# Performance work log

Hardware: AMD Instinct MI355X
Metric: run time of the kernel (lower is better)

The kernel has to match this reference:

```python
import jax, jax.numpy as jnp
import numpy as np

D_MODEL = 1024
N_LAYER = 4
D_INNER = 2048   # expand * d_model
D_STATE = 16
D_CONV = 4
DT_RANK = 64     # ceil(d_model / 16)
B, L = 2, 1024
EPS = 1e-5


def setup_inputs() -> dict:
    key = jax.random.key(0)
    ks = jax.random.split(key, 10)
    nl = N_LAYER
    def nrm(k, shape, s=0.02):
        return jax.random.normal(k, shape, jnp.float32) * s
    A_log = jnp.broadcast_to(jnp.log(jnp.arange(1, D_STATE + 1, dtype=jnp.float32)),
                             (nl, D_INNER, D_STATE)) + jnp.zeros((nl, D_INNER, D_STATE), jnp.float32)
    return {
        "hidden_states": jax.random.normal(ks[0], (B, L, D_MODEL), jnp.float32),
        "in_proj_w": nrm(ks[1], (nl, 2 * D_INNER, D_MODEL)),
        "conv_w": nrm(ks[2], (nl, D_INNER, D_CONV), 0.1),
        "conv_b": nrm(ks[3], (nl, D_INNER), 0.02),
        "x_proj_w": nrm(ks[4], (nl, DT_RANK + 2 * D_STATE, D_INNER)),
        "dt_proj_w": nrm(ks[5], (nl, D_INNER, DT_RANK), DT_RANK ** -0.5),
        "dt_proj_b": jnp.log(jnp.expm1(jax.random.uniform(ks[6], (nl, D_INNER), jnp.float32, 1e-3, 0.1))),
        "A_log": A_log,
        "D": jnp.ones((nl, D_INNER), jnp.float32),
        "out_proj_w": nrm(ks[7], (nl, D_MODEL, D_INNER)),
        "norm_w": jnp.ones((nl, D_MODEL), jnp.float32),
        "norm_b": jnp.zeros((nl, D_MODEL), jnp.float32),
        "normf_w": jnp.ones((D_MODEL,), jnp.float32),
        "normf_b": jnp.zeros((D_MODEL,), jnp.float32),
    }


def _layernorm(x, w, b):
    mu = x.mean(-1, keepdims=True)
    var = ((x - mu) ** 2).mean(-1, keepdims=True)
    return (x - mu) * jax.lax.rsqrt(var + EPS) * w + b


def _mamba(h, iw, cw, cb, xw, dw, db, Alog, Dp, ow):
    Bn, Ln, _ = h.shape
    xz = jnp.einsum('bld,ed->ble', h, iw)          # [B,L,2*d_inner]
    x, z = jnp.split(xz, 2, axis=-1)
    # depthwise causal conv1d over time, kernel size D_CONV
    xp = jnp.pad(x, ((0, 0), (D_CONV - 1, 0), (0, 0)))
    xc = sum(xp[:, k:k + Ln, :] * cw[:, k] for k in range(D_CONV)) + cb
    x = jax.nn.silu(xc)
    dbl = jnp.einsum('bld,ed->ble', x, xw)         # [B,L,dt_rank+2*d_state]
    dt = dbl[..., :DT_RANK]
    Bm = dbl[..., DT_RANK:DT_RANK + D_STATE]
    Cm = dbl[..., DT_RANK + D_STATE:]
    dt = jax.nn.softplus(jnp.einsum('blr,dr->bld', dt, dw) + db)  # [B,L,d_inner]
    A = -jnp.exp(Alog)                              # [d_inner,d_state]

    def step(hc, inp):
        dt_t, B_t, C_t, x_t = inp                   # [B,d],[B,s],[B,s],[B,d]
        dA = jnp.exp(dt_t[:, :, None] * A)
        hc = hc * dA + (dt_t * x_t)[:, :, None] * B_t[:, None, :]
        y_t = jnp.einsum('bds,bs->bd', hc, C_t)
        return hc, y_t

    h0 = jnp.zeros((Bn, D_INNER, D_STATE), x.dtype)
    xs = (dt.transpose(1, 0, 2), Bm.transpose(1, 0, 2),
          Cm.transpose(1, 0, 2), x.transpose(1, 0, 2))
    _, ys = jax.lax.scan(step, h0, xs)              # ys: [L,B,d_inner]
    y = ys.transpose(1, 0, 2) + x * Dp
    y = y * jax.nn.silu(z)
    return jnp.einsum('bld,ed->ble', y, ow)


def reference(hidden_states, in_proj_w, conv_w, conv_b, x_proj_w, dt_proj_w,
              dt_proj_b, A_log, D, out_proj_w, norm_w, norm_b, normf_w, normf_b):
    hs = hidden_states
    residual = None
    for i in range(N_LAYER):
        residual = hs if residual is None else hs + residual
        hs = _layernorm(residual, norm_w[i], norm_b[i])
        hs = _mamba(hs, in_proj_w[i], conv_w[i], conv_b[i], x_proj_w[i],
                    dt_proj_w[i], dt_proj_b[i], A_log[i], D[i], out_proj_w[i])
    residual = hs + residual
    return _layernorm(residual, normf_w, normf_b)
```

## Files before the change

### kernel.cpp

```cpp
#include <hip/hip_runtime.h>
#include <math.h>

#define D_MODEL 1024
#define D_INNER 2048
#define D_STATE 16
#define D_CONV  4
#define DT_RANK 64
#define NB      2
#define LSEQ    1024
#define NROWS   (NB * LSEQ)
#define LN_EPS  1e-5f
#define N_LAYER 4
#define NCHUNK  32
#define TCH     (LSEQ / NCHUNK)

__device__ inline unsigned bfbits(float f) {
    unsigned u = __float_as_uint(f);
    return (u + 0x7fffu + ((u >> 16) & 1u)) >> 16;
}

#define GLOAD_LDS16(gp, lp) \
    __builtin_amdgcn_global_load_lds( \
        (const __attribute__((address_space(1))) void*)(gp), \
        (__attribute__((address_space(3))) void*)(lp), 16, 0, 0)

__device__ inline float wave_sum(float s) {
    #pragma unroll
    for (int m = 1; m < 64; m <<= 1) s += __shfl_xor(s, m, 64);
    return s;
}

__device__ inline void add_ln_body(int row, int tid,
                                   const float* __restrict__ add,
                                   float* __restrict__ residual,
                                   const float* __restrict__ w, const float* __restrict__ b,
                                   void* __restrict__ out, int first, int bf16out,
                                   float* red)
{
    size_t base = (size_t)row * D_MODEL + tid * 4;

    float4 v = *(const float4*)(add + base);
    if (!first) {
        float4 r = *(const float4*)(residual + base);
        v.x += r.x; v.y += r.y; v.z += r.z; v.w += r.w;
    }
    *(float4*)(residual + base) = v;

    float s = v.x + v.y + v.z + v.w;
    s = wave_sum(s);
    if ((tid & 63) == 0) red[tid >> 6] = s;
    __syncthreads();
    float mu = (red[0] + red[1] + red[2] + red[3]) * (1.0f / D_MODEL);

    float dx = v.x - mu, dy = v.y - mu, dz = v.z - mu, dw2 = v.w - mu;
    float s2 = dx*dx + dy*dy + dz*dz + dw2*dw2;
    s2 = wave_sum(s2);
    if ((tid & 63) == 0) red[4 + (tid >> 6)] = s2;
    __syncthreads();
    float var = (red[4] + red[5] + red[6] + red[7]) * (1.0f / D_MODEL);
    float rs = rsqrtf(var + LN_EPS);

    float4 wv = *(const float4*)(w + tid * 4);
    float4 bv = *(const float4*)(b + tid * 4);
    float4 o;
    o.x = dx  * rs * wv.x + bv.x;
    o.y = dy  * rs * wv.y + bv.y;
    o.z = dz  * rs * wv.z + bv.z;
    o.w = dw2 * rs * wv.w + bv.w;
    if (bf16out) {
        ushort4 ov;
        ov.x = (unsigned short)bfbits(o.x);
        ov.y = (unsigned short)bfbits(o.y);
        ov.z = (unsigned short)bfbits(o.z);
        ov.w = (unsigned short)bfbits(o.w);
        *(ushort4*)((unsigned short*)out + base) = ov;
    } else {
        *(float4*)((float*)out + base) = o;
    }
}

__global__ __launch_bounds__(256)
void add_ln_kernel(const float* __restrict__ add, float* __restrict__ residual,
                   const float* __restrict__ w, const float* __restrict__ b,
                   void* __restrict__ out, int first, int bf16out)
{
    __shared__ float red[8];
    add_ln_body(blockIdx.x, threadIdx.x, add, residual, w, b, out, first, bf16out, red);
}

__global__ __launch_bounds__(256)
void f32_to_bf16_kernel(const float* __restrict__ src, unsigned short* __restrict__ dst)
{
    int i = blockIdx.x * 256 + threadIdx.x;
    float4 v = *(const float4*)(src + (size_t)i * 4);
    ushort4 o;
    o.x = (unsigned short)bfbits(v.x);
    o.y = (unsigned short)bfbits(v.y);
    o.z = (unsigned short)bfbits(v.z);
    o.w = (unsigned short)bfbits(v.w);
    *(ushort4*)(dst + (size_t)i * 4) = o;
}

__device__ inline void hl_split4(float4 v, ushort4* h4, ushort4* l4)
{
    ushort4 h, l;
    float f;
    h.x = (unsigned short)bfbits(v.x); f = __uint_as_float((unsigned)h.x << 16); l.x = (unsigned short)bfbits(v.x - f);
    h.y = (unsigned short)bfbits(v.y); f = __uint_as_float((unsigned)h.y << 16); l.y = (unsigned short)bfbits(v.y - f);
    h.z = (unsigned short)bfbits(v.z); f = __uint_as_float((unsigned)h.z << 16); l.z = (unsigned short)bfbits(v.z - f);
    h.w = (unsigned short)bfbits(v.w); f = __uint_as_float((unsigned)h.w << 16); l.w = (unsigned short)bfbits(v.w - f);
    *h4 = h; *l4 = l;
}

__global__ __launch_bounds__(256)
void lnprep_kernel(const float* __restrict__ add, float* __restrict__ residual,
                   const float* __restrict__ w, const float* __restrict__ b,
                   unsigned short* __restrict__ ln_out, int first,
                   const float* __restrict__ iw, unsigned short* __restrict__ wbuf_in,
                   const float* __restrict__ xw, unsigned short* __restrict__ xwh,
                   unsigned short* __restrict__ xwl,
                   const float* __restrict__ dw, unsigned short* __restrict__ dwh,
                   unsigned short* __restrict__ dwl,
                   float* __restrict__ dbl)
{
    __shared__ float red[8];
    int b0 = blockIdx.x;
    int tid = threadIdx.x;
    if (b0 < 2048) {
        add_ln_body(b0, tid, add, residual, w, b, ln_out, first, 1, red);
    } else if (b0 < 6144) {
        int i = (b0 - 2048) * 256 + tid;
        float4 v = *(const float4*)(iw + (size_t)i * 4);
        ushort4 o;
        o.x = (unsigned short)bfbits(v.x);
        o.y = (unsigned short)bfbits(v.y);
        o.z = (unsigned short)bfbits(v.z);
        o.w = (unsigned short)bfbits(v.w);
        *(ushort4*)(wbuf_in + (size_t)i * 4) = o;
    } else if (b0 < 6336) {
        int i = (b0 - 6144) * 256 + tid;
        float4 v = *(const float4*)(xw + (size_t)i * 4);
        hl_split4(v, (ushort4*)(xwh + (size_t)i * 4), (ushort4*)(xwl + (size_t)i * 4));
    } else if (b0 < 6464) {
        int i = (b0 - 6336) * 256 + tid;
        float4 v = *(const float4*)(dw + (size_t)i * 4);
        hl_split4(v, (ushort4*)(dwh + (size_t)i * 4), (ushort4*)(dwl + (size_t)i * 4));
    } else {
        int i = (b0 - 6464) * 256 + tid;
        *(float4*)(dbl + (size_t)i * 4) = make_float4(0.f, 0.f, 0.f, 0.f);
    }
}

using bf16x8 = __attribute__((ext_vector_type(8))) short;
using f32x4  = __attribute__((ext_vector_type(4))) float;

#define BBM 128
#define BBN 128
#define BBK 64

__global__ __launch_bounds__(256)
void gemm_bf16_nt(const unsigned short* __restrict__ A, const unsigned short* __restrict__ Bw,
                  float* __restrict__ C, int M, int N, int K)
{
    __shared__ unsigned short As[BBM * BBK];
    __shared__ unsigned short Bs[BBN * BBK];

    int tid = threadIdx.x;
    int m0 = blockIdx.y * BBM, n0 = blockIdx.x * BBN;
    int lane = tid & 63, w = tid >> 6;
    int wm = (w >> 1) * 64, wn = (w & 1) * 64;
    int lm = lane & 15, q = lane >> 4;

    int lrow8 = lane >> 3;
    int scol  = ((lane & 7) ^ lrow8) * 8;

    f32x4 acc[4][4] = {};

    for (int k0 = 0; k0 < K; k0 += BBK) {
        #pragma unroll
        for (int j = 0; j < 4; ++j) {
            int rbase = w * 32 + j * 8;
            GLOAD_LDS16(A + (size_t)(m0 + rbase + lrow8) * K + k0 + scol,
                        &As[rbase * BBK]);
        }
        #pragma unroll
        for (int j = 0; j < 4; ++j) {
            int rbase = w * 32 + j * 8;
            GLOAD_LDS16(Bw + (size_t)(n0 + rbase + lrow8) * K + k0 + scol,
                        &Bs[rbase * BBK]);
        }
        __syncthreads();
        #pragma unroll
        for (int kk = 0; kk < BBK; kk += 32) {
            bf16x8 af[4], bf[4];
            #pragma unroll
            for (int i = 0; i < 4; ++i) {
                int row = wm + i * 16 + lm;
                int col = (kk + q * 8) ^ ((row & 7) << 3);
                af[i] = *(const bf16x8*)&As[row * BBK + col];
            }
            #pragma unroll
            for (int j = 0; j < 4; ++j) {
                int row = wn + j * 16 + lm;
                int col = (kk + q * 8) ^ ((row & 7) << 3);
                bf[j] = *(const bf16x8*)&Bs[row * BBK + col];
            }
            #pragma unroll
            for (int i = 0; i < 4; ++i)
                #pragma unroll
                for (int j = 0; j < 4; ++j)
                    acc[i][j] = __builtin_amdgcn_mfma_f32_16x16x32_bf16(
                        af[i], bf[j], acc[i][j], 0, 0, 0);
        }
        __syncthreads();
    }

    #pragma unroll
    for (int i = 0; i < 4; ++i)
        #pragma unroll
        for (int j = 0; j < 4; ++j)
            #pragma unroll
            for (int r = 0; r < 4; ++r) {
                int row = m0 + wm + i * 16 + q * 4 + r;
                int col = n0 + wn + j * 16 + lm;
                C[(size_t)row * N + col] = acc[i][j][r];
            }
}

__global__ __launch_bounds__(256)
void xproj_hl(const unsigned short* __restrict__ Ah, const unsigned short* __restrict__ Al,
              const unsigned short* __restrict__ Bh, const unsigned short* __restrict__ Bl,
              float* __restrict__ C)
{
    int tid = threadIdx.x;
    int lane = tid & 63, w = tid >> 6;
    int lm = lane & 15, q = lane >> 4;
    int m0 = blockIdx.x * 32;
    int kb = blockIdx.y * 256;

    int wm = (w & 1) * 16;
    int wn = (w >> 1) * 48;

    size_t arow = (size_t)(m0 + wm + lm) * 2048;

    f32x4 acc[3] = {};

    #pragma unroll 2
    for (int kc = 0; kc < 8; ++kc) {
        int k = kb + kc * 32 + q * 8;
        bf16x8 ah = *(const bf16x8*)&Ah[arow + k];
        bf16x8 al = *(const bf16x8*)&Al[arow + k];
        #pragma unroll
        for (int j = 0; j < 3; ++j) {
            size_t brow = (size_t)(wn + j * 16 + lm) * 2048;
            bf16x8 bh = *(const bf16x8*)&Bh[brow + k];
            bf16x8 bl = *(const bf16x8*)&Bl[brow + k];
            acc[j] = __builtin_amdgcn_mfma_f32_16x16x32_bf16(al, bh, acc[j], 0, 0, 0);
            acc[j] = __builtin_amdgcn_mfma_f32_16x16x32_bf16(ah, bl, acc[j], 0, 0, 0);
            acc[j] = __builtin_amdgcn_mfma_f32_16x16x32_bf16(ah, bh, acc[j], 0, 0, 0);
        }
    }

    #pragma unroll
    for (int j = 0; j < 3; ++j) {
        int col = wn + j * 16 + lm;
        #pragma unroll
        for (int r = 0; r < 4; ++r) {
            int row = m0 + wm + q * 4 + r;
            atomicAdd(&C[(size_t)row * 96 + col], acc[j][r]);
        }
    }
}

__global__ __launch_bounds__(256)
void dtproj_hl(const float* __restrict__ dbl,
               const unsigned short* __restrict__ Bh, const unsigned short* __restrict__ Bl,
               const float* __restrict__ bias, float* __restrict__ dtb)
{
    int tid = threadIdx.x;
    int lane = tid & 63, w = tid >> 6;
    int lm = lane & 15, q = lane >> 4;
    int n0 = blockIdx.x * 128;
    int m0 = blockIdx.y * 64;

    const float* arow = dbl + (size_t)(m0 + w * 16 + lm) * 96;

    f32x4 acc[8] = {};

    #pragma unroll
    for (int kc = 0; kc < 2; ++kc) {
        int k = kc * 32 + q * 8;
        float4 v0 = *(const float4*)(arow + k);
        float4 v1 = *(const float4*)(arow + k + 4);
        float vv[8] = {v0.x, v0.y, v0.z, v0.w, v1.x, v1.y, v1.z, v1.w};
        bf16x8 ah, al;
        #pragma unroll
        for (int s = 0; s < 8; ++s) {
            unsigned hb = bfbits(vv[s]);
            ah[s] = (short)hb;
            al[s] = (short)bfbits(vv[s] - __uint_as_float(hb << 16));
        }
        #pragma unroll
        for (int j = 0; j < 8; ++j) {
            size_t brow = (size_t)(n0 + j * 16 + lm) * 64;
            bf16x8 bh = *(const bf16x8*)&Bh[brow + k];
            bf16x8 bl = *(const bf16x8*)&Bl[brow + k];
            acc[j] = __builtin_amdgcn_mfma_f32_16x16x32_bf16(al, bh, acc[j], 0, 0, 0);
            acc[j] = __builtin_amdgcn_mfma_f32_16x16x32_bf16(ah, bl, acc[j], 0, 0, 0);
            acc[j] = __builtin_amdgcn_mfma_f32_16x16x32_bf16(ah, bh, acc[j], 0, 0, 0);
        }
    }

    #pragma unroll
    for (int j = 0; j < 8; ++j) {
        int col = n0 + j * 16 + lm;
        float bv = bias[col];
        #pragma unroll
        for (int r = 0; r < 4; ++r) {
            int row = m0 + w * 16 + q * 4 + r;
            float v = acc[j][r] + bv;
            v = (v > 20.f) ? v : log1pf(__expf(v));
            dtb[(size_t)row * D_INNER + col] = v;
        }
    }
}

__global__ __launch_bounds__(256)
void conv_silu_kernel(const float* __restrict__ xz, const float* __restrict__ cw,
                      const float* __restrict__ cb, float* __restrict__ xc,
                      unsigned short* __restrict__ xch, unsigned short* __restrict__ xcl)
{
    int idx = blockIdx.x * 256 + threadIdx.x;
    int d  = idx & (D_INNER - 1);
    int t  = (idx >> 11) & (LSEQ - 1);
    int bb = idx >> 21;

    const float* xcol = xz + (size_t)bb * LSEQ * 2 * D_INNER + d;
    float acc = cb[d];
    #pragma unroll
    for (int k = 0; k < D_CONV; ++k) {
        int tt = t + k - (D_CONV - 1);
        if (tt >= 0) acc += xcol[(size_t)tt * 2 * D_INNER] * cw[d * D_CONV + k];
    }
    acc = acc / (1.f + __expf(-acc));
    xc[idx] = acc;
    unsigned hb = bfbits(acc);
    xch[idx] = (unsigned short)hb;
    float hf = __uint_as_float(hb << 16);
    xcl[idx] = (unsigned short)bfbits(acc - hf);
}

#define UNPK4(dst, off, v) { dst[(off)+0]=(v).x; dst[(off)+1]=(v).y; \
                             dst[(off)+2]=(v).z; dst[(off)+3]=(v).w; }

__global__ __launch_bounds__(256)
void scan_pass1(const float* __restrict__ dtb, const float* __restrict__ xc,
                const float* __restrict__ dbl, const float* __restrict__ Alog,
                float* __restrict__ aPbuf, float* __restrict__ bAbuf)
{
    int tid  = threadIdx.x;
    int half = tid & 1;
    int blk  = blockIdx.x;
    int dg   = blk & 15;
    int c    = (blk >> 4) & (NCHUNK - 1);
    int bb   = blk >> 9;
    int d    = dg * 128 + (tid >> 1);

    float A[8];
    {
        const float* pA = Alog + (size_t)d * D_STATE + half * 8;
        float4 v0 = *(const float4*)pA;
        float4 v1 = *(const float4*)(pA + 4);
        A[0] = -__expf(v0.x); A[1] = -__expf(v0.y);
        A[2] = -__expf(v0.z); A[3] = -__expf(v0.w);
        A[4] = -__expf(v1.x); A[5] = -__expf(v1.y);
        A[6] = -__expf(v1.z); A[7] = -__expf(v1.w);
    }

    size_t rowbase = (size_t)bb * LSEQ + (size_t)c * TCH;
    const float* pdt = dtb + rowbase * D_INNER + d;
    const float* pxc = xc  + rowbase * D_INNER + d;
    const float* pbc = dbl + rowbase * 96 + DT_RANK + half * 8;

    float aP[8] = {1.f,1.f,1.f,1.f,1.f,1.f,1.f,1.f};
    float bA[8] = {0.f,0.f,0.f,0.f,0.f,0.f,0.f,0.f};

    float  dtE = pdt[0], xvE = pxc[0];
    float4 BE0 = *(const float4*)pbc;
    float4 BE1 = *(const float4*)(pbc + 4);
    float  dtO = pdt[D_INNER], xvO = pxc[D_INNER];
    float4 BO0 = *(const float4*)(pbc + 96);
    float4 BO1 = *(const float4*)(pbc + 96 + 4);

    const float* qdtE = pdt + 2 * D_INNER;
    const float* qdtO = pdt + 3 * D_INNER;
    const float* qxcE = pxc + 2 * D_INNER;
    const float* qxcO = pxc + 3 * D_INNER;
    const float* qbcE = pbc + 2 * 96;
    const float* qbcO = pbc + 3 * 96;

#define P1_STEP(DT, XV, B0, B1) { \
        float B[8]; UNPK4(B, 0, B0) UNPK4(B, 4, B1) \
        float dtx = (DT) * (XV); \
        _Pragma("unroll") \
        for (int s = 0; s < 8; ++s) { \
            float a = __expf((DT) * A[s]); \
            aP[s] *= a; \
            bA[s] = bA[s] * a + dtx * B[s]; \
        } }

    for (int t = 0; t < TCH - 4; t += 2) {
        float  dtEn = qdtE[0], xvEn = qxcE[0];
        float4 BE0n = *(const float4*)qbcE;
        float4 BE1n = *(const float4*)(qbcE + 4);
        float  dtOn = qdtO[0], xvOn = qxcO[0];
        float4 BO0n = *(const float4*)qbcO;
        float4 BO1n = *(const float4*)(qbcO + 4);
        qdtE += 2 * D_INNER; qdtO += 2 * D_INNER;
        qxcE += 2 * D_INNER; qxcO += 2 * D_INNER;
        qbcE += 192; qbcO += 192;

        P1_STEP(dtE, xvE, BE0, BE1)
        P1_STEP(dtO, xvO, BO0, BO1)

        dtE = dtEn; xvE = xvEn; BE0 = BE0n; BE1 = BE1n;
        dtO = dtOn; xvO = xvOn; BO0 = BO0n; BO1 = BO1n;
    }
    {
        float  dtEn = qdtE[0], xvEn = qxcE[0];
        float4 BE0n = *(const float4*)qbcE;
        float4 BE1n = *(const float4*)(qbcE + 4);
        float  dtOn = qdtO[0], xvOn = qxcO[0];
        float4 BO0n = *(const float4*)qbcO;
        float4 BO1n = *(const float4*)(qbcO + 4);

        P1_STEP(dtE, xvE, BE0, BE1)
        P1_STEP(dtO, xvO, BO0, BO1)

        dtE = dtEn; xvE = xvEn; BE0 = BE0n; BE1 = BE1n;
        dtO = dtOn; xvO = xvOn; BO0 = BO0n; BO1 = BO1n;
    }
    {
        P1_STEP(dtE, xvE, BE0, BE1)
        P1_STEP(dtO, xvO, BO0, BO1)
    }
#undef P1_STEP

    float* pa = aPbuf + ((size_t)(bb * NCHUNK + c) * D_INNER + d) * D_STATE + half * 8;
    float* pb = bAbuf + ((size_t)(bb * NCHUNK + c) * D_INNER + d) * D_STATE + half * 8;
    *(float4*)(pa + 0) = make_float4(aP[0], aP[1], aP[2], aP[3]);
    *(float4*)(pa + 4) = make_float4(aP[4], aP[5], aP[6], aP[7]);
    *(float4*)(pb + 0) = make_float4(bA[0], bA[1], bA[2], bA[3]);
    *(float4*)(pb + 4) = make_float4(bA[4], bA[5], bA[6], bA[7]);
}

__global__ __launch_bounds__(256)
void scan_prefix(const float* __restrict__ aPbuf, float* __restrict__ bAbuf)
{
    int idx = blockIdx.x * 256 + threadIdx.x;
    int sp = idx & 7;
    int d  = (idx >> 3) & (D_INNER - 1);
    int bb = idx >> 14;

    size_t o = ((size_t)(bb * NCHUNK) * D_INNER + d) * D_STATE + sp * 2;
    const size_t stride = (size_t)D_INNER * D_STATE;
    float h0 = 0.f, h1 = 0.f;
    #pragma unroll 4
    for (int c = 0; c < NCHUNK; ++c) {
        float2 a2 = *(const float2*)(aPbuf + o);
        float2 b2 = *(const float2*)(bAbuf + o);
        *(float2*)(bAbuf + o) = make_float2(h0, h1);
        h0 = h0 * a2.x + b2.x;
        h1 = h1 * a2.y + b2.y;
        o += stride;
    }
}

__global__ __launch_bounds__(256)
void scan_pass2(const float* __restrict__ dtb, const float* __restrict__ xc,
                const float* __restrict__ dbl, const float* __restrict__ xz,
                const float* __restrict__ Alog, const float* __restrict__ Dp,
                const float* __restrict__ bAbuf,
                unsigned short* __restrict__ y)
{
    int tid  = threadIdx.x;
    int half = tid & 1;
    int blk  = blockIdx.x;
    int dg   = blk & 15;
    int c    = (blk >> 4) & (NCHUNK - 1);
    int bb   = blk >> 9;
    int d    = dg * 128 + (tid >> 1);

    float A[8];
    {
        const float* pA = Alog + (size_t)d * D_STATE + half * 8;
        float4 v0 = *(const float4*)pA;
        float4 v1 = *(const float4*)(pA + 4);
        A[0] = -__expf(v0.x); A[1] = -__expf(v0.y);
        A[2] = -__expf(v0.z); A[3] = -__expf(v0.w);
        A[4] = -__expf(v1.x); A[5] = -__expf(v1.y);
        A[6] = -__expf(v1.z); A[7] = -__expf(v1.w);
    }
    float Dd = Dp[d];

    float h[8];
    {
        const float* ph = bAbuf + ((size_t)(bb * NCHUNK + c) * D_INNER + d) * D_STATE + half * 8;
        float4 h0v = *(const float4*)(ph + 0);
        float4 h1v = *(const float4*)(ph + 4);
        UNPK4(h, 0, h0v) UNPK4(h, 4, h1v)
    }

    size_t rowbase = (size_t)bb * LSEQ + (size_t)c * TCH;
    const float* pdt = dtb + rowbase * D_INNER + d;
    const float* pxc = xc  + rowbase * D_INNER + d;
    const float* pz  = xz  + rowbase * 2 * D_INNER + D_INNER + d;
    const float* pbc = dbl + rowbase * 96 + DT_RANK + half * 8;
    unsigned short* qyE = y + rowbase * D_INNER + d;
    unsigned short* qyO = qyE + D_INNER;

    float  dtE = pdt[0], xvE = pxc[0], zvE = pz[0];
    float4 BE0 = *(const float4*)pbc;
    float4 BE1 = *(const float4*)(pbc + 4);
    float4 CE0 = *(const float4*)(pbc + 16);
    float4 CE1 = *(const float4*)(pbc + 20);
    float  dtO = pdt[D_INNER], xvO = pxc[D_INNER], zvO = pz[2 * D_INNER];
    float4 BO0 = *(const float4*)(pbc + 96);
    float4 BO1 = *(const float4*)(pbc + 96 + 4);
    float4 CO0 = *(const float4*)(pbc + 96 + 16);
    float4 CO1 = *(const float4*)(pbc + 96 + 20);

    const float* qdtE = pdt + 2 * D_INNER;
    const float* qdtO = pdt + 3 * D_INNER;
    const float* qxcE = pxc + 2 * D_INNER;
    const float* qxcO = pxc + 3 * D_INNER;
    const float* qzE  = pz  + 4 * D_INNER;
    const float* qzO  = pz  + 6 * D_INNER;
    const float* qbcE = pbc + 2 * 96;
    const float* qbcO = pbc + 3 * 96;

#define P2_STEP(DT, XV, ZV, B0, B1, C0, C1, PY) { \
        float B[8], C[8]; \
        UNPK4(B, 0, B0) UNPK4(B, 4, B1) \
        UNPK4(C, 0, C0) UNPK4(C, 4, C1) \
        float dtx = (DT) * (XV); \
        float p = 0.f; \
        _Pragma("unroll") \
        for (int s = 0; s < 8; ++s) { \
            float a = __expf((DT) * A[s]); \
            h[s] = h[s] * a + dtx * B[s]; \
            p += h[s] * C[s]; \
        } \
        p += __shfl_xor(p, 1, 2); \
        if (half == 0) { \
            float sz = (ZV) / (1.f + __expf(-(ZV))); \
            *(PY) = (unsigned short)bfbits((p + (XV) * Dd) * sz); \
        } }

    for (int t = 0; t < TCH - 4; t += 2) {
        float  dtEn = qdtE[0], xvEn = qxcE[0], zvEn = qzE[0];
        float4 BE0n = *(const float4*)qbcE;
        float4 BE1n = *(const float4*)(qbcE + 4);
        float4 CE0n = *(const float4*)(qbcE + 16);
        float4 CE1n = *(const float4*)(qbcE + 20);
        float  dtOn = qdtO[0], xvOn = qxcO[0], zvOn = qzO[0];
        float4 BO0n = *(const float4*)qbcO;
        float4 BO1n = *(const float4*)(qbcO + 4);
        float4 CO0n = *(const float4*)(qbcO + 16);
        float4 CO1n = *(const float4*)(qbcO + 20);
        qdtE += 2 * D_INNER; qdtO += 2 * D_INNER;
        qxcE += 2 * D_INNER; qxcO += 2 * D_INNER;
        qzE  += 4 * D_INNER; qzO  += 4 * D_INNER;
        qbcE += 192; qbcO += 192;

        P2_STEP(dtE, xvE, zvE, BE0, BE1, CE0, CE1, qyE)
        qyE += 2 * D_INNER;
        P2_STEP(dtO, xvO, zvO, BO0, BO1, CO0, CO1, qyO)
        qyO += 2 * D_INNER;

        dtE = dtEn; xvE = xvEn; zvE = zvEn;
        BE0 = BE0n; BE1 = BE1n; CE0 = CE0n; CE1 = CE1n;
        dtO = dtOn; xvO = xvOn; zvO = zvOn;
        BO0 = BO0n; BO1 = BO1n; CO0 = CO0n; CO1 = CO1n;
    }
    {
        float  dtEn = qdtE[0], xvEn = qxcE[0], zvEn = qzE[0];
        float4 BE0n = *(const float4*)qbcE;
        float4 BE1n = *(const float4*)(qbcE + 4);
        float4 CE0n = *(const float4*)(qbcE + 16);
        float4 CE1n = *(const float4*)(qbcE + 20);
        float  dtOn = qdtO[0], xvOn = qxcO[0], zvOn = qzO[0];
        float4 BO0n = *(const float4*)qbcO;
        float4 BO1n = *(const float4*)(qbcO + 4);
        float4 CO0n = *(const float4*)(qbcO + 16);
        float4 CO1n = *(const float4*)(qbcO + 20);

        P2_STEP(dtE, xvE, zvE, BE0, BE1, CE0, CE1, qyE)
        qyE += 2 * D_INNER;
        P2_STEP(dtO, xvO, zvO, BO0, BO1, CO0, CO1, qyO)
        qyO += 2 * D_INNER;

        dtE = dtEn; xvE = xvEn; zvE = zvEn;
        BE0 = BE0n; BE1 = BE1n; CE0 = CE0n; CE1 = CE1n;
        dtO = dtOn; xvO = xvOn; zvO = zvOn;
        BO0 = BO0n; BO1 = BO1n; CO0 = CO0n; CO1 = CO1n;
    }
    {
        P2_STEP(dtE, xvE, zvE, BE0, BE1, CE0, CE1, qyE)
        P2_STEP(dtO, xvO, zvO, BO0, BO1, CO0, CO1, qyO)
    }
#undef P2_STEP
}

extern "C" void kernel_launch(void* const* d_in, const int* in_sizes, int n_in,
                              void* d_out, int out_size, void* d_ws, size_t ws_size,
                              hipStream_t stream)
{
    const float* h_in  = (const float*)d_in[0];
    const float* iw    = (const float*)d_in[1];
    const float* cw    = (const float*)d_in[2];
    const float* cb    = (const float*)d_in[3];
    const float* xw    = (const float*)d_in[4];
    const float* dw    = (const float*)d_in[5];
    const float* db    = (const float*)d_in[6];
    const float* Alog  = (const float*)d_in[7];
    const float* Dp    = (const float*)d_in[8];
    const float* ow    = (const float*)d_in[9];
    const float* nw    = (const float*)d_in[10];
    const float* nb    = (const float*)d_in[11];
    const float* nfw   = (const float*)d_in[12];
    const float* nfb   = (const float*)d_in[13];

    float* ws = (float*)d_ws;
    float* residual = ws;
    float* hs       = residual + 2097152;
    float* xz       = hs + 2097152;
    float* xc       = xz + 8388608;
    float* dtb      = xc + 4194304;
    float* dbl      = dtb + 4194304;
    float* y        = dbl + 196608;

    float* aPbuf = hs;
    float* bAbuf = y + 2097152;

    unsigned short* wbuf_in  = (unsigned short*)y;
    unsigned short* hs_bf16  = (unsigned short*)(y + 2097152);
    unsigned short* y_bf16   = (unsigned short*)y;
    unsigned short* xc_hi    = (unsigned short*)y;
    unsigned short* xc_lo    = (unsigned short*)(y + 2097152);
    unsigned short* xwp_hi   = (unsigned short*)hs;
    unsigned short* xwp_lo   = (unsigned short*)(hs + 98304);
    unsigned short* dwp_hi   = (unsigned short*)(hs + 196608);
    unsigned short* dwp_lo   = (unsigned short*)(hs + 262144);
    unsigned short* wbuf_out = (unsigned short*)dtb;

    const float* cur_add = h_in;
    for (int i = 0; i < N_LAYER; ++i) {
        lnprep_kernel<<<6656, 256, 0, stream>>>(
            cur_add, residual, nw + i * D_MODEL, nb + i * D_MODEL, hs_bf16, i == 0,
            iw + (size_t)i * 2 * D_INNER * D_MODEL, wbuf_in,
            xw + (size_t)i * 96 * D_INNER, xwp_hi, xwp_lo,
            dw + (size_t)i * D_INNER * DT_RANK, dwp_hi, dwp_lo,
            dbl);
        gemm_bf16_nt<<<dim3(2 * D_INNER / BBN, NROWS / BBM), 256, 0, stream>>>(
            hs_bf16, wbuf_in, xz, NROWS, 2 * D_INNER, D_MODEL);
        conv_silu_kernel<<<NB * LSEQ * D_INNER / 256, 256, 0, stream>>>(
            xz, cw + (size_t)i * D_INNER * D_CONV, cb + i * D_INNER, xc, xc_hi, xc_lo);
        xproj_hl<<<dim3(NROWS / 32, 8), 256, 0, stream>>>(
            xc_hi, xc_lo, xwp_hi, xwp_lo, dbl);
        dtproj_hl<<<dim3(D_INNER / 128, NROWS / 64), 256, 0, stream>>>(
            dbl, dwp_hi, dwp_lo, db + i * D_INNER, dtb);
        scan_pass1<<<NB * NCHUNK * (D_INNER / 128), 256, 0, stream>>>(
            dtb, xc, dbl, Alog + (size_t)i * D_INNER * D_STATE, aPbuf, bAbuf);
        scan_prefix<<<(NB * D_INNER * 8) / 256, 256, 0, stream>>>(aPbuf, bAbuf);
        scan_pass2<<<NB * NCHUNK * (D_INNER / 128), 256, 0, stream>>>(
            dtb, xc, dbl, xz, Alog + (size_t)i * D_INNER * D_STATE, Dp + i * D_INNER,
            bAbuf, y_bf16);
        f32_to_bf16_kernel<<<(D_MODEL * D_INNER) / 1024, 256, 0, stream>>>(
            ow + (size_t)i * D_MODEL * D_INNER, wbuf_out);
        gemm_bf16_nt<<<dim3(D_MODEL / BBN, NROWS / BBM), 256, 0, stream>>>(
            y_bf16, wbuf_out, hs, NROWS, D_MODEL, D_INNER);
        cur_add = hs;
    }
    add_ln_kernel<<<NROWS, 256, 0, stream>>>(hs, residual, nfw, nfb, d_out, 0, 0);
}
```

Measured before the change: 942.2 us.

## Double-buffer the bf16 GEMM and template its tile shape per projection

The bf16 MFMA GEMM becomes a templated kernel with two LDS buffers. The next K-tile is issued with global_load_lds while the current tile is multiplied, leaving one barrier per iteration instead of two. The in_proj launch switches to 128x64 tiles and the out_proj launch to 64x64 tiles, so more blocks fill the device, especially out_proj, which had only 128 blocks. Costs: twice the LDS per block, and smaller tiles that load more data from global memory per FLOP.

```diff
diff --git a/kernel.cpp b/kernel.cpp
--- a/kernel.cpp
+++ b/kernel.cpp
@@ -154,61 +154,68 @@
 using bf16x8 = __attribute__((ext_vector_type(8))) short;
 using f32x4  = __attribute__((ext_vector_type(4))) float;
 
-#define BBM 128
-#define BBN 128
-#define BBK 64
-
-__global__ __launch_bounds__(256)
-void gemm_bf16_nt(const unsigned short* __restrict__ A, const unsigned short* __restrict__ Bw,
-                  float* __restrict__ C, int M, int N, int K)
-{
-    __shared__ unsigned short As[BBM * BBK];
-    __shared__ unsigned short Bs[BBN * BBK];
+template<int BM, int BN>
+__global__ __launch_bounds__(256)
+void gemm_bf16_dbuf(const unsigned short* __restrict__ A, const unsigned short* __restrict__ Bw,
+                    float* __restrict__ C, int M, int N, int K)
+{
+    constexpr int MF = BM / 32;
+    constexpr int NF = BN / 32;
+    __shared__ unsigned short As[2][BM * 64];
+    __shared__ unsigned short Bs[2][BN * 64];
 
     int tid = threadIdx.x;
-    int m0 = blockIdx.y * BBM, n0 = blockIdx.x * BBN;
+    int m0 = blockIdx.y * BM, n0 = blockIdx.x * BN;
     int lane = tid & 63, w = tid >> 6;
-    int wm = (w >> 1) * 64, wn = (w & 1) * 64;
+    int wm = (w >> 1) * (BM / 2), wn = (w & 1) * (BN / 2);
     int lm = lane & 15, q = lane >> 4;
 
     int lrow8 = lane >> 3;
     int scol  = ((lane & 7) ^ lrow8) * 8;
 
-    f32x4 acc[4][4] = {};
-
-    for (int k0 = 0; k0 < K; k0 += BBK) {
-        #pragma unroll
-        for (int j = 0; j < 4; ++j) {
-            int rbase = w * 32 + j * 8;
-            GLOAD_LDS16(A + (size_t)(m0 + rbase + lrow8) * K + k0 + scol,
-                        &As[rbase * BBK]);
-        }
-        #pragma unroll
-        for (int j = 0; j < 4; ++j) {
-            int rbase = w * 32 + j * 8;
-            GLOAD_LDS16(Bw + (size_t)(n0 + rbase + lrow8) * K + k0 + scol,
-                        &Bs[rbase * BBK]);
-        }
-        __syncthreads();
-        #pragma unroll
-        for (int kk = 0; kk < BBK; kk += 32) {
-            bf16x8 af[4], bf[4];
+    f32x4 acc[MF][NF] = {};
+
+    auto STAGE = [&](int buf, int k0) {
+        #pragma unroll
+        for (int j = 0; j < MF; ++j) {
+            int rb = w * (BM / 4) + j * 8;
+            GLOAD_LDS16(A + (size_t)(m0 + rb + lrow8) * K + k0 + scol,
+                        &As[buf][rb * 64]);
+        }
+        #pragma unroll
+        for (int j = 0; j < NF; ++j) {
+            int rb = w * (BN / 4) + j * 8;
+            GLOAD_LDS16(Bw + (size_t)(n0 + rb + lrow8) * K + k0 + scol,
+                        &Bs[buf][rb * 64]);
+        }
+    };
+
+    STAGE(0, 0);
+    __syncthreads();
+
+    int nk = K >> 6;
+    for (int kt = 0; kt < nk; ++kt) {
+        int cur = kt & 1;
+        if (kt + 1 < nk) STAGE(cur ^ 1, (kt + 1) << 6);
+        #pragma unroll
+        for (int kk = 0; kk < 64; kk += 32) {
+            bf16x8 af[MF], bf[NF];
             #pragma unroll
-            for (int i = 0; i < 4; ++i) {
+            for (int i = 0; i < MF; ++i) {
                 int row = wm + i * 16 + lm;
                 int col = (kk + q * 8) ^ ((row & 7) << 3);
-                af[i] = *(const bf16x8*)&As[row * BBK + col];
+                af[i] = *(const bf16x8*)&As[cur][row * 64 + col];
             }
             #pragma unroll
-            for (int j = 0; j < 4; ++j) {
+            for (int j = 0; j < NF; ++j) {
                 int row = wn + j * 16 + lm;
                 int col = (kk + q * 8) ^ ((row & 7) << 3);
-                bf[j] = *(const bf16x8*)&Bs[row * BBK + col];
+                bf[j] = *(const bf16x8*)&Bs[cur][row * 64 + col];
             }
             #pragma unroll
-            for (int i = 0; i < 4; ++i)
+            for (int i = 0; i < MF; ++i)
                 #pragma unroll
-                for (int j = 0; j < 4; ++j)
+                for (int j = 0; j < NF; ++j)
                     acc[i][j] = __builtin_amdgcn_mfma_f32_16x16x32_bf16(
                         af[i], bf[j], acc[i][j], 0, 0, 0);
         }
@@ -216,9 +223,9 @@
     }
 
     #pragma unroll
-    for (int i = 0; i < 4; ++i)
-        #pragma unroll
-        for (int j = 0; j < 4; ++j)
+    for (int i = 0; i < MF; ++i)
+        #pragma unroll
+        for (int j = 0; j < NF; ++j)
             #pragma unroll
             for (int r = 0; r < 4; ++r) {
                 int row = m0 + wm + i * 16 + q * 4 + r;
@@ -662,7 +669,7 @@
             xw + (size_t)i * 96 * D_INNER, xwp_hi, xwp_lo,
             dw + (size_t)i * D_INNER * DT_RANK, dwp_hi, dwp_lo,
             dbl);
-        gemm_bf16_nt<<<dim3(2 * D_INNER / BBN, NROWS / BBM), 256, 0, stream>>>(
+        gemm_bf16_dbuf<128, 64><<<dim3(2 * D_INNER / 64, NROWS / 128), 256, 0, stream>>>(
             hs_bf16, wbuf_in, xz, NROWS, 2 * D_INNER, D_MODEL);
         conv_silu_kernel<<<NB * LSEQ * D_INNER / 256, 256, 0, stream>>>(
             xz, cw + (size_t)i * D_INNER * D_CONV, cb + i * D_INNER, xc, xc_hi, xc_lo);
@@ -678,7 +685,7 @@
             bAbuf, y_bf16);
         f32_to_bf16_kernel<<<(D_MODEL * D_INNER) / 1024, 256, 0, stream>>>(
             ow + (size_t)i * D_MODEL * D_INNER, wbuf_out);
-        gemm_bf16_nt<<<dim3(D_MODEL / BBN, NROWS / BBM), 256, 0, stream>>>(
+        gemm_bf16_dbuf<64, 64><<<dim3(D_MODEL / 64, NROWS / 64), 256, 0, stream>>>(
             y_bf16, wbuf_out, hs, NROWS, D_MODEL, D_INNER);
         cur_add = hs;
     }
```

Measured after the change: 899.6 us. -4.5%, faster.
